# Kernel optimization log

Hardware: AMD Instinct MI355X
Metric: run time of the kernel (lower is better)

Reference implementation:

```python
import jax, jax.numpy as jnp
import numpy as np

B, N, D, O = 16384, 784, 8, 10   # batch, num_sites, bond_dim, output_dim
LABEL = N // 2                   # 392
L_LEFT = LABEL - 1               # sites 1..391 -> 391 mid tensors
L_RIGHT = N - 2 - LABEL          # sites 393..782 -> 390 mid tensors


def setup_inputs() -> dict:
    key = jax.random.key(0)
    k0, k1, k2, k3, k4, k5 = jax.random.split(key, 6)
    x = jax.random.uniform(k0, (B, N, 1), dtype=jnp.float32)
    # scale mid tensors so the 784-site matrix product stays O(1):
    # per-site variance multiplier ~ D * var(w) * E[phi^2]*2 with E[phi^2]=1/3
    s_mid = (3.0 / (2.0 * D)) ** 0.5
    w0 = jax.random.normal(k1, (2, D), dtype=jnp.float32) * 1.2
    W_left = jax.random.normal(k2, (L_LEFT, D, 2, D), dtype=jnp.float32) * s_mid
    w_label = jax.random.normal(k3, (D, 2, D, O), dtype=jnp.float32) * s_mid
    W_right = jax.random.normal(k4, (L_RIGHT, D, 2, D), dtype=jnp.float32) * s_mid
    w_last = jax.random.normal(k5, (D, 2), dtype=jnp.float32) * 1.2
    return {"x": x, "w0": w0, "W_left": W_left, "w_label": w_label,
            "W_right": W_right, "w_last": w_last}


def reference(x, w0, W_left, w_label, W_right, w_last):
    p = jnp.squeeze(x, axis=-1)                       # [B, N]
    phi = jnp.stack([1.0 - p, p], axis=-1)            # [B, N, 2] feature map

    # site 0: [B,2] x [2,D] -> left boundary vector [B,D]
    v = jnp.einsum('bf,fd->bd', phi[:, 0], w0)

    def step_left(v, xw):
        phi_i, w_i = xw                               # [B,2], [D,2,D]
        return jnp.einsum('bd,dfe,bf->be', v, w_i, phi_i), None

    phiL = jnp.transpose(phi[:, 1:LABEL], (1, 0, 2))  # [L_LEFT, B, 2]
    v, _ = jax.lax.scan(step_left, v, (phiL, W_left))

    # label site: [B,D] x [D,2,D,O] x [B,2] -> [B,D,O]
    v = jnp.einsum('bd,dfeo,bf->beo', v, w_label, phi[:, LABEL])

    def step_right(v, xw):
        phi_i, w_i = xw
        return jnp.einsum('bdo,dfe,bf->beo', v, w_i, phi_i), None

    phiR = jnp.transpose(phi[:, LABEL + 1:N - 1], (1, 0, 2))  # [L_RIGHT, B, 2]
    v, _ = jax.lax.scan(step_right, v, (phiR, W_right))

    # last site: right boundary vector [B,D], then close the chain -> [B,O]
    r = jnp.einsum('bf,df->bd', phi[:, N - 1], w_last)
    return jnp.einsum('bdo,bd->bo', v, r)
```

## Files before the change

### kernel.cpp

```cpp
#include <hip/hip_runtime.h>


#define NSITES 784
#define DIM    8
#define ODIM   10
#define LABEL  392
#define WST    160
#define XST    20

#define QP_X1 0xB1
#define QP_X2 0x4E
#define QP_X3 0x1B
#define RHM   0x141

template <int CTRL>
__device__ __forceinline__ float dppf(float v) {
    const int vi = __float_as_int(v);
    return __int_as_float(__builtin_amdgcn_update_dpp(vi, vi, CTRL, 0xF, 0xF, false));
}

__device__ __forceinline__ float site_step(float v, float p, const float* wsite) {
    const float4 w00 = *(const float4*)(wsite + 0);
    const float4 w01 = *(const float4*)(wsite + 4);
    const float4 w10 = *(const float4*)(wsite + 8);
    const float4 w11 = *(const float4*)(wsite + 12);
    const float t1 = dppf<QP_X1>(v);
    const float t2 = dppf<QP_X2>(v);
    const float t3 = dppf<QP_X3>(v);
    const float t7 = dppf<RHM>(v);
    const float t6 = dppf<QP_X1>(t7);
    const float t5 = dppf<QP_X2>(t7);
    const float t4 = dppf<QP_X3>(t7);
    float a0 = v * w00.x;
    float a1 = v * w10.x;
    a0 = fmaf(t1, w00.y, a0);  a1 = fmaf(t1, w10.y, a1);
    a0 = fmaf(t2, w00.z, a0);  a1 = fmaf(t2, w10.z, a1);
    a0 = fmaf(t3, w00.w, a0);  a1 = fmaf(t3, w10.w, a1);
    a0 = fmaf(t4, w01.x, a0);  a1 = fmaf(t4, w11.x, a1);
    a0 = fmaf(t5, w01.y, a0);  a1 = fmaf(t5, w11.y, a1);
    a0 = fmaf(t6, w01.z, a0);  a1 = fmaf(t6, w11.z, a1);
    a0 = fmaf(t7, w01.w, a0);  a1 = fmaf(t7, w11.w, a1);
    return fmaf(1.0f - p, a0, p * a1);
}

__global__ __launch_bounds__(512, 4) void mps_fused(
    const float* __restrict__ x,
    const float* __restrict__ w0,
    const float* __restrict__ Wl,
    const float* __restrict__ wlab,
    const float* __restrict__ Wr,
    const float* __restrict__ wlast,
    float* __restrict__ out)
{
    __shared__ float wb[2][2][16 * WST];
    __shared__ float xb[2][2][32 * XST];
    __shared__ float wl[1280];
    __shared__ float vout[2][256];

    const int tid  = threadIdx.x;
    const int side = tid >> 8;
    const int stid = tid & 255;
    const int g    = stid >> 3;
    const int e    = stid & 7;
    const int b0   = blockIdx.x * 32;

    if (tid < 320)
        *(float4*)&wl[tid * 4] = *(const float4*)&wlab[tid * 4];

    auto stage = [&](int bufi, int c, int nt) {
        float* wdst = wb[side][bufi];
        float* xdst = xb[side][bufi];
        if (side == 0) {
            #pragma unroll
            for (int r = 0; r < 2; ++r) {
                const int cid = stid + 256 * r;
                const int s   = cid >> 5;
                const int u   = cid & 31;
                const int d   = u >> 2;
                const int f   = (u >> 1) & 1;
                const int e0  = (u & 1) * 4;
                if (s < nt) {
                    const float4 w = *(const float4*)(Wl + (size_t)(c * 16 + s) * 128 + d * 16 + f * 8 + e0);
                    float* dst = wdst + s * WST + f * 8;
                    dst[(e0 + 0) * 20 + ((e0 + 0) ^ d)] = w.x;
                    dst[(e0 + 1) * 20 + ((e0 + 1) ^ d)] = w.y;
                    dst[(e0 + 2) * 20 + ((e0 + 2) ^ d)] = w.z;
                    dst[(e0 + 3) * 20 + ((e0 + 3) ^ d)] = w.w;
                }
            }
            #pragma unroll
            for (int r = 0; r < 2; ++r) {
                const int cid = stid + 256 * r;
                const int s   = cid >> 5;
                const int g2  = cid & 31;
                if (s < nt)
                    xdst[g2 * XST + s] = x[(size_t)(b0 + g2) * NSITES + 1 + c * 16 + s];
            }
        } else {
            #pragma unroll
            for (int r = 0; r < 2; ++r) {
                const int cid = stid + 256 * r;
                const int s   = cid >> 5;
                const int u   = cid & 31;
                const int d   = u >> 2;
                const int k   = u & 3;
                const int f   = k >> 1;
                const int e0  = (k & 1) * 4;
                if (s < nt) {
                    const float4 w = *(const float4*)(Wr + (size_t)(389 - c * 16 - s) * 128 + u * 4);
                    float* dst = wdst + s * WST + d * 20 + f * 8;
                    dst[(e0 + 0) ^ d] = w.x;
                    dst[(e0 + 1) ^ d] = w.y;
                    dst[(e0 + 2) ^ d] = w.z;
                    dst[(e0 + 3) ^ d] = w.w;
                }
            }
            #pragma unroll
            for (int r = 0; r < 2; ++r) {
                const int cid = stid + 256 * r;
                const int s   = cid >> 5;
                const int g2  = cid & 31;
                if (s < nt)
                    xdst[g2 * XST + s] = x[(size_t)(b0 + g2) * NSITES + 782 - c * 16 - s];
            }
        }
    };

    float v;
    if (side == 0) {
        const float p = x[(size_t)(b0 + g) * NSITES + 0];
        v = fmaf(1.0f - p, w0[e], p * w0[DIM + e]);
    } else {
        const float p = x[(size_t)(b0 + g) * NSITES + (NSITES - 1)];
        v = fmaf(1.0f - p, wlast[e * 2], p * wlast[e * 2 + 1]);
    }

    stage(0, 0, 16);
    int buf = 0;

    const float* wp0 = &wb[side][0][e * 20];
    const float* wp1 = &wb[side][1][e * 20];
    const float* xp0 = &xb[side][0][g * XST];
    const float* xp1 = &xb[side][1][g * XST];

    #pragma unroll 1
    for (int c = 0; c < 24; ++c) {
        __syncthreads();
        if (c < 23) stage(buf ^ 1, c + 1, 16);
        else        stage(buf ^ 1, 24, side == 0 ? 7 : 6);
        const float* wp = buf ? wp1 : wp0;
        const float* xp = buf ? xp1 : xp0;
        #pragma unroll
        for (int jb = 0; jb < 4; ++jb) {
            const float4 xq = *(const float4*)(xp + jb * 4);
            #pragma unroll
            for (int jj = 0; jj < 4; ++jj) {
                const int   j = jb * 4 + jj;
                const float p = (jj == 0) ? xq.x : (jj == 1) ? xq.y : (jj == 2) ? xq.z : xq.w;
                v = site_step(v, p, wp + j * WST);
            }
        }
        buf ^= 1;
    }

    __syncthreads();
    {
        const int nt = side == 0 ? 7 : 6;
        const float* wp = buf ? wp1 : wp0;
        const float* xp = buf ? xp1 : xp0;
        for (int j = 0; j < nt; ++j)
            v = site_step(v, xp[j], wp + j * WST);
    }

    vout[side][stid] = v;
    __syncthreads();

    if (tid < 320) {
        const int bl = tid / 10;
        const int o  = tid - bl * 10;
        const float p = x[(size_t)(b0 + bl) * NSITES + LABEL];
        const float q = 1.0f - p;
        const float* vl = &vout[0][bl * 8];
        const float* rv = &vout[1][bl * 8];
        float acc = 0.0f;
        #pragma unroll
        for (int d = 0; d < DIM; ++d) {
            const float vld = vl[d];
            #pragma unroll
            for (int ee = 0; ee < DIM; ++ee) {
                const float m = fmaf(q, wl[((d * 2 + 0) * DIM + ee) * ODIM + o],
                                     p * wl[((d * 2 + 1) * DIM + ee) * ODIM + o]);
                acc = fmaf(vld * rv[ee], m, acc);
            }
        }
        out[(size_t)(b0 + bl) * ODIM + o] = acc;
    }
}

extern "C" void kernel_launch(void* const* d_in, const int* in_sizes, int n_in,
                              void* d_out, int out_size, void* d_ws, size_t ws_size,
                              hipStream_t stream) {
    const float* x     = (const float*)d_in[0];
    const float* w0    = (const float*)d_in[1];
    const float* Wl    = (const float*)d_in[2];
    const float* wlab  = (const float*)d_in[3];
    const float* Wr    = (const float*)d_in[4];
    const float* wlast = (const float*)d_in[5];

    mps_fused<<<512, 512, 0, stream>>>(x, w0, Wl, wlab, Wr, wlast, (float*)d_out);
}
```

Measured before the change: 185.2 us.

## Process four batch rows per thread and prefetch stages through registers

Each thread now carries four independent chain vectors (64 batch rows per block, 256 threads, 256 blocks), so the site weights loaded from shared memory are reused across four rows and the four DPP/FMA chains can interleave to hide latency. The global loads for the next stage go into registers before the compute and are written to shared memory after it, which overlaps memory traffic with arithmetic. The final interpolation is rewritten as a single fma form. The cost is fewer resident threads per CU (launch bounds 256,1 and only 256 blocks) and more register pressure, so occupancy and latency hiding across waves drop.

```diff
diff --git a/kernel.cpp b/kernel.cpp
--- a/kernel.cpp
+++ b/kernel.cpp
@@ -6,6 +6,7 @@
 #define ODIM   10
 #define LABEL  392
 #define WST    160
+#define CST    20
 #define XST    20
 
 #define QP_X1 0xB1
@@ -19,11 +20,9 @@
     return __int_as_float(__builtin_amdgcn_update_dpp(vi, vi, CTRL, 0xF, 0xF, false));
 }
 
-__device__ __forceinline__ float site_step(float v, float p, const float* wsite) {
-    const float4 w00 = *(const float4*)(wsite + 0);
-    const float4 w01 = *(const float4*)(wsite + 4);
-    const float4 w10 = *(const float4*)(wsite + 8);
-    const float4 w11 = *(const float4*)(wsite + 12);
+struct W4 { float4 w00, w01, w10, w11; };
+
+__device__ __forceinline__ float site_step(float v, float p, const W4& w) {
     const float t1 = dppf<QP_X1>(v);
     const float t2 = dppf<QP_X2>(v);
     const float t3 = dppf<QP_X3>(v);
@@ -31,19 +30,19 @@
     const float t6 = dppf<QP_X1>(t7);
     const float t5 = dppf<QP_X2>(t7);
     const float t4 = dppf<QP_X3>(t7);
-    float a0 = v * w00.x;
-    float a1 = v * w10.x;
-    a0 = fmaf(t1, w00.y, a0);  a1 = fmaf(t1, w10.y, a1);
-    a0 = fmaf(t2, w00.z, a0);  a1 = fmaf(t2, w10.z, a1);
-    a0 = fmaf(t3, w00.w, a0);  a1 = fmaf(t3, w10.w, a1);
-    a0 = fmaf(t4, w01.x, a0);  a1 = fmaf(t4, w11.x, a1);
-    a0 = fmaf(t5, w01.y, a0);  a1 = fmaf(t5, w11.y, a1);
-    a0 = fmaf(t6, w01.z, a0);  a1 = fmaf(t6, w11.z, a1);
-    a0 = fmaf(t7, w01.w, a0);  a1 = fmaf(t7, w11.w, a1);
-    return fmaf(1.0f - p, a0, p * a1);
-}
-
-__global__ __launch_bounds__(512, 4) void mps_fused(
+    float a0 = v * w.w00.x;
+    float a1 = v * w.w10.x;
+    a0 = fmaf(t1, w.w00.y, a0);  a1 = fmaf(t1, w.w10.y, a1);
+    a0 = fmaf(t2, w.w00.z, a0);  a1 = fmaf(t2, w.w10.z, a1);
+    a0 = fmaf(t3, w.w00.w, a0);  a1 = fmaf(t3, w.w10.w, a1);
+    a0 = fmaf(t4, w.w01.x, a0);  a1 = fmaf(t4, w.w11.x, a1);
+    a0 = fmaf(t5, w.w01.y, a0);  a1 = fmaf(t5, w.w11.y, a1);
+    a0 = fmaf(t6, w.w01.z, a0);  a1 = fmaf(t6, w.w11.z, a1);
+    a0 = fmaf(t7, w.w01.w, a0);  a1 = fmaf(t7, w.w11.w, a1);
+    return fmaf(p, a1 - a0, a0);
+}
+
+__global__ __launch_bounds__(256, 1) void mps_fused(
     const float* __restrict__ x,
     const float* __restrict__ w0,
     const float* __restrict__ Wl,
@@ -53,131 +52,204 @@
     float* __restrict__ out)
 {
     __shared__ float wb[2][2][16 * WST];
-    __shared__ float xb[2][2][32 * XST];
+    __shared__ float xb[2][2][64 * XST];
     __shared__ float wl[1280];
-    __shared__ float vout[2][256];
+    __shared__ float vout[2][512];
 
     const int tid  = threadIdx.x;
-    const int side = tid >> 8;
-    const int stid = tid & 255;
-    const int g    = stid >> 3;
-    const int e    = stid & 7;
-    const int b0   = blockIdx.x * 32;
-
-    if (tid < 320)
-        *(float4*)&wl[tid * 4] = *(const float4*)&wlab[tid * 4];
-
-    auto stage = [&](int bufi, int c, int nt) {
+    const int side = tid >> 7;
+    const int stid = tid & 127;
+    const int w    = stid >> 6;
+    const int lane = stid & 63;
+    const int g    = lane >> 3;
+    const int e    = lane & 7;
+    const int b0   = blockIdx.x * 64;
+
+    for (int k = tid; k < 320; k += 256)
+        *(float4*)&wl[k * 4] = *(const float4*)&wlab[k * 4];
+
+    float4 wr[4];
+    float  xr[8];
+
+    auto stage_load = [&](int c, int nt) {
+        if (side == 0) {
+            #pragma unroll
+            for (int r = 0; r < 4; ++r) {
+                const int cid = stid + 128 * r;
+                const int s   = cid >> 5;
+                const int u   = cid & 31;
+                if (s < nt)
+                    wr[r] = *(const float4*)(Wl + (size_t)(c * 16 + s) * 128
+                                             + (u >> 2) * 16 + ((u >> 1) & 1) * 8 + (u & 1) * 4);
+            }
+            #pragma unroll
+            for (int r = 0; r < 8; ++r) {
+                const int cid = stid + 128 * r;
+                const int bl  = cid >> 4;
+                const int sx  = cid & 15;
+                if (sx < nt)
+                    xr[r] = x[(size_t)(b0 + bl) * NSITES + 1 + c * 16 + sx];
+            }
+        } else {
+            #pragma unroll
+            for (int r = 0; r < 4; ++r) {
+                const int cid = stid + 128 * r;
+                const int s   = cid >> 5;
+                const int u   = cid & 31;
+                if (s < nt)
+                    wr[r] = *(const float4*)(Wr + (size_t)(389 - c * 16 - s) * 128 + u * 4);
+            }
+            #pragma unroll
+            for (int r = 0; r < 8; ++r) {
+                const int cid = stid + 128 * r;
+                const int bl  = cid >> 4;
+                const int sx  = cid & 15;
+                if (sx < nt)
+                    xr[r] = x[(size_t)(b0 + bl) * NSITES + 782 - c * 16 - sx];
+            }
+        }
+    };
+
+    auto stage_write = [&](int bufi, int nt) {
         float* wdst = wb[side][bufi];
         float* xdst = xb[side][bufi];
         if (side == 0) {
             #pragma unroll
-            for (int r = 0; r < 2; ++r) {
-                const int cid = stid + 256 * r;
+            for (int r = 0; r < 4; ++r) {
+                const int cid = stid + 128 * r;
                 const int s   = cid >> 5;
                 const int u   = cid & 31;
                 const int d   = u >> 2;
                 const int f   = (u >> 1) & 1;
                 const int e0  = (u & 1) * 4;
                 if (s < nt) {
-                    const float4 w = *(const float4*)(Wl + (size_t)(c * 16 + s) * 128 + d * 16 + f * 8 + e0);
                     float* dst = wdst + s * WST + f * 8;
-                    dst[(e0 + 0) * 20 + ((e0 + 0) ^ d)] = w.x;
-                    dst[(e0 + 1) * 20 + ((e0 + 1) ^ d)] = w.y;
-                    dst[(e0 + 2) * 20 + ((e0 + 2) ^ d)] = w.z;
-                    dst[(e0 + 3) * 20 + ((e0 + 3) ^ d)] = w.w;
+                    dst[(e0 + 0) * CST + ((e0 + 0) ^ d)] = wr[r].x;
+                    dst[(e0 + 1) * CST + ((e0 + 1) ^ d)] = wr[r].y;
+                    dst[(e0 + 2) * CST + ((e0 + 2) ^ d)] = wr[r].z;
+                    dst[(e0 + 3) * CST + ((e0 + 3) ^ d)] = wr[r].w;
                 }
             }
-            #pragma unroll
-            for (int r = 0; r < 2; ++r) {
-                const int cid = stid + 256 * r;
-                const int s   = cid >> 5;
-                const int g2  = cid & 31;
-                if (s < nt)
-                    xdst[g2 * XST + s] = x[(size_t)(b0 + g2) * NSITES + 1 + c * 16 + s];
-            }
         } else {
             #pragma unroll
-            for (int r = 0; r < 2; ++r) {
-                const int cid = stid + 256 * r;
+            for (int r = 0; r < 4; ++r) {
+                const int cid = stid + 128 * r;
                 const int s   = cid >> 5;
                 const int u   = cid & 31;
                 const int d   = u >> 2;
-                const int k   = u & 3;
-                const int f   = k >> 1;
-                const int e0  = (k & 1) * 4;
+                const int k2  = u & 3;
+                const int f   = k2 >> 1;
+                const int e0  = (k2 & 1) * 4;
                 if (s < nt) {
-                    const float4 w = *(const float4*)(Wr + (size_t)(389 - c * 16 - s) * 128 + u * 4);
-                    float* dst = wdst + s * WST + d * 20 + f * 8;
-                    dst[(e0 + 0) ^ d] = w.x;
-                    dst[(e0 + 1) ^ d] = w.y;
-                    dst[(e0 + 2) ^ d] = w.z;
-                    dst[(e0 + 3) ^ d] = w.w;
+                    float* dst = wdst + s * WST + d * CST + f * 8;
+                    dst[(e0 + 0) ^ d] = wr[r].x;
+                    dst[(e0 + 1) ^ d] = wr[r].y;
+                    dst[(e0 + 2) ^ d] = wr[r].z;
+                    dst[(e0 + 3) ^ d] = wr[r].w;
                 }
             }
-            #pragma unroll
-            for (int r = 0; r < 2; ++r) {
-                const int cid = stid + 256 * r;
-                const int s   = cid >> 5;
-                const int g2  = cid & 31;
-                if (s < nt)
-                    xdst[g2 * XST + s] = x[(size_t)(b0 + g2) * NSITES + 782 - c * 16 - s];
-            }
+        }
+        #pragma unroll
+        for (int r = 0; r < 8; ++r) {
+            const int cid = stid + 128 * r;
+            const int bl  = cid >> 4;
+            const int sx  = cid & 15;
+            if (sx < nt)
+                xdst[bl * XST + sx] = xr[r];
         }
     };
 
-    float v;
+    float vv[4];
     if (side == 0) {
-        const float p = x[(size_t)(b0 + g) * NSITES + 0];
-        v = fmaf(1.0f - p, w0[e], p * w0[DIM + e]);
+        #pragma unroll
+        for (int k = 0; k < 4; ++k) {
+            const int bl  = w * 32 + k * 8 + g;
+            const float p = x[(size_t)(b0 + bl) * NSITES];
+            vv[k] = fmaf(1.0f - p, w0[e], p * w0[DIM + e]);
+        }
     } else {
-        const float p = x[(size_t)(b0 + g) * NSITES + (NSITES - 1)];
-        v = fmaf(1.0f - p, wlast[e * 2], p * wlast[e * 2 + 1]);
-    }
-
-    stage(0, 0, 16);
+        #pragma unroll
+        for (int k = 0; k < 4; ++k) {
+            const int bl  = w * 32 + k * 8 + g;
+            const float p = x[(size_t)(b0 + bl) * NSITES + (NSITES - 1)];
+            vv[k] = fmaf(1.0f - p, wlast[e * 2], p * wlast[e * 2 + 1]);
+        }
+    }
+
+    const int nt_tail = side ? 6 : 7;
+
+    stage_load(0, 16);
+    stage_write(0, 16);
     int buf = 0;
 
-    const float* wp0 = &wb[side][0][e * 20];
-    const float* wp1 = &wb[side][1][e * 20];
-    const float* xp0 = &xb[side][0][g * XST];
-    const float* xp1 = &xb[side][1][g * XST];
+    auto compute16 = [&](int bufi) {
+        const float* wp = &wb[side][bufi][e * CST];
+        const float* xp = &xb[side][bufi][(w * 32 + g) * XST];
+        #pragma unroll
+        for (int jb = 0; jb < 4; ++jb) {
+            float4 xq[4];
+            #pragma unroll
+            for (int k = 0; k < 4; ++k)
+                xq[k] = *(const float4*)(xp + k * 8 * XST + jb * 4);
+            #pragma unroll
+            for (int jj = 0; jj < 4; ++jj) {
+                const int j = jb * 4 + jj;
+                W4 wv;
+                wv.w00 = *(const float4*)(wp + j * WST + 0);
+                wv.w01 = *(const float4*)(wp + j * WST + 4);
+                wv.w10 = *(const float4*)(wp + j * WST + 8);
+                wv.w11 = *(const float4*)(wp + j * WST + 12);
+                #pragma unroll
+                for (int k = 0; k < 4; ++k) {
+                    const float p = (jj == 0) ? xq[k].x : (jj == 1) ? xq[k].y
+                                  : (jj == 2) ? xq[k].z : xq[k].w;
+                    vv[k] = site_step(vv[k], p, wv);
+                }
+            }
+        }
+    };
 
     #pragma unroll 1
-    for (int c = 0; c < 24; ++c) {
+    for (int c = 0; c < 23; ++c) {
         __syncthreads();
-        if (c < 23) stage(buf ^ 1, c + 1, 16);
-        else        stage(buf ^ 1, 24, side == 0 ? 7 : 6);
-        const float* wp = buf ? wp1 : wp0;
-        const float* xp = buf ? xp1 : xp0;
-        #pragma unroll
-        for (int jb = 0; jb < 4; ++jb) {
-            const float4 xq = *(const float4*)(xp + jb * 4);
-            #pragma unroll
-            for (int jj = 0; jj < 4; ++jj) {
-                const int   j = jb * 4 + jj;
-                const float p = (jj == 0) ? xq.x : (jj == 1) ? xq.y : (jj == 2) ? xq.z : xq.w;
-                v = site_step(v, p, wp + j * WST);
-            }
-        }
+        stage_load(c + 1, 16);
+        compute16(buf);
+        __builtin_amdgcn_sched_barrier(0);
+        stage_write(buf ^ 1, 16);
         buf ^= 1;
     }
+
+    __syncthreads();
+    stage_load(24, nt_tail);
+    compute16(buf);
+    __builtin_amdgcn_sched_barrier(0);
+    stage_write(buf ^ 1, nt_tail);
+    buf ^= 1;
 
     __syncthreads();
     {
-        const int nt = side == 0 ? 7 : 6;
-        const float* wp = buf ? wp1 : wp0;
-        const float* xp = buf ? xp1 : xp0;
-        for (int j = 0; j < nt; ++j)
-            v = site_step(v, xp[j], wp + j * WST);
-    }
-
-    vout[side][stid] = v;
+        const float* wp = &wb[side][buf][e * CST];
+        const float* xp = &xb[side][buf][(w * 32 + g) * XST];
+        for (int j = 0; j < nt_tail; ++j) {
+            W4 wv;
+            wv.w00 = *(const float4*)(wp + j * WST + 0);
+            wv.w01 = *(const float4*)(wp + j * WST + 4);
+            wv.w10 = *(const float4*)(wp + j * WST + 8);
+            wv.w11 = *(const float4*)(wp + j * WST + 12);
+            #pragma unroll
+            for (int k = 0; k < 4; ++k)
+                vv[k] = site_step(vv[k], xp[k * 8 * XST + j], wv);
+        }
+    }
+
+    #pragma unroll
+    for (int k = 0; k < 4; ++k)
+        vout[side][(w * 32 + k * 8 + g) * 8 + e] = vv[k];
     __syncthreads();
 
-    if (tid < 320) {
-        const int bl = tid / 10;
-        const int o  = tid - bl * 10;
+    for (int idx = tid; idx < 640; idx += 256) {
+        const int bl = idx / 10;
+        const int o  = idx - bl * 10;
         const float p = x[(size_t)(b0 + bl) * NSITES + LABEL];
         const float q = 1.0f - p;
         const float* vl = &vout[0][bl * 8];
@@ -200,6 +272,7 @@
 extern "C" void kernel_launch(void* const* d_in, const int* in_sizes, int n_in,
                               void* d_out, int out_size, void* d_ws, size_t ws_size,
                               hipStream_t stream) {
+    (void)in_sizes; (void)n_in; (void)d_ws; (void)ws_size; (void)out_size;
     const float* x     = (const float*)d_in[0];
     const float* w0    = (const float*)d_in[1];
     const float* Wl    = (const float*)d_in[2];
@@ -207,5 +280,5 @@
     const float* Wr    = (const float*)d_in[4];
     const float* wlast = (const float*)d_in[5];
 
-    mps_fused<<<512, 512, 0, stream>>>(x, w0, Wl, wlab, Wr, wlast, (float*)d_out);
-}
+    mps_fused<<<256, 256, 0, stream>>>(x, w0, Wl, wlab, Wr, wlast, (float*)d_out);
+}
```

Result: slower. 195.6 us (+5.6%).

## Process two batch rows per thread with packed FP32 math and register-staged prefetch

Applied to the files above, without the earlier changes.

Each thread now carries two batch rows in a float2 and uses v_pk_mul/v_pk_fma packed FP32 instructions. Weights are duplicated into pairs in shared memory so one packed operand serves both rows. Global loads for the next chunk go into registers before compute and are written to LDS afterwards, separated by a sched_barrier, to overlap memory latency with the serial chain. Blocks now cover 64 rows (grid halved, launch bounds 512,2), which doubles the DPP work per thread and the LDS footprint and may reduce occupancy.

```diff
diff --git a/kernel.cpp b/kernel.cpp
--- a/kernel.cpp
+++ b/kernel.cpp
@@ -5,45 +5,75 @@
 #define DIM    8
 #define ODIM   10
 #define LABEL  392
-#define WST    160
-#define XST    20
-
-#define QP_X1 0xB1
-#define QP_X2 0x4E
-#define QP_X3 0x1B
-#define RHM   0x141
-
-template <int CTRL>
-__device__ __forceinline__ float dppf(float v) {
-    const int vi = __float_as_int(v);
-    return __int_as_float(__builtin_amdgcn_update_dpp(vi, vi, CTRL, 0xF, 0xF, false));
-}
-
-__device__ __forceinline__ float site_step(float v, float p, const float* wsite) {
-    const float4 w00 = *(const float4*)(wsite + 0);
-    const float4 w01 = *(const float4*)(wsite + 4);
-    const float4 w10 = *(const float4*)(wsite + 8);
-    const float4 w11 = *(const float4*)(wsite + 12);
-    const float t1 = dppf<QP_X1>(v);
-    const float t2 = dppf<QP_X2>(v);
-    const float t3 = dppf<QP_X3>(v);
-    const float t7 = dppf<RHM>(v);
-    const float t6 = dppf<QP_X1>(t7);
-    const float t5 = dppf<QP_X2>(t7);
-    const float t4 = dppf<QP_X3>(t7);
-    float a0 = v * w00.x;
-    float a1 = v * w10.x;
-    a0 = fmaf(t1, w00.y, a0);  a1 = fmaf(t1, w10.y, a1);
-    a0 = fmaf(t2, w00.z, a0);  a1 = fmaf(t2, w10.z, a1);
-    a0 = fmaf(t3, w00.w, a0);  a1 = fmaf(t3, w10.w, a1);
-    a0 = fmaf(t4, w01.x, a0);  a1 = fmaf(t4, w11.x, a1);
-    a0 = fmaf(t5, w01.y, a0);  a1 = fmaf(t5, w11.y, a1);
-    a0 = fmaf(t6, w01.z, a0);  a1 = fmaf(t6, w11.z, a1);
-    a0 = fmaf(t7, w01.w, a0);  a1 = fmaf(t7, w11.w, a1);
-    return fmaf(1.0f - p, a0, p * a1);
-}
-
-__global__ __launch_bounds__(512, 4) void mps_fused(
+#define WST2   288
+#define CST2   36
+#define XQST   34
+
+typedef float v2f __attribute__((ext_vector_type(2)));
+
+__device__ __forceinline__ float dpp_x1(float s) {
+    float d; asm("v_mov_b32_dpp %0, %1 quad_perm:[1,0,3,2] row_mask:0xf bank_mask:0xf"
+                 : "=v"(d) : "v"(s)); return d;
+}
+__device__ __forceinline__ float dpp_x2(float s) {
+    float d; asm("v_mov_b32_dpp %0, %1 quad_perm:[2,3,0,1] row_mask:0xf bank_mask:0xf"
+                 : "=v"(d) : "v"(s)); return d;
+}
+__device__ __forceinline__ float dpp_x3(float s) {
+    float d; asm("v_mov_b32_dpp %0, %1 quad_perm:[3,2,1,0] row_mask:0xf bank_mask:0xf"
+                 : "=v"(d) : "v"(s)); return d;
+}
+__device__ __forceinline__ float dpp_x7(float s) {
+    float d; asm("v_mov_b32_dpp %0, %1 row_half_mirror row_mask:0xf bank_mask:0xf"
+                 : "=v"(d) : "v"(s)); return d;
+}
+
+__device__ __forceinline__ v2f pk_mul(v2f a, v2f b) {
+    v2f d; asm("v_pk_mul_f32 %0, %1, %2" : "=v"(d) : "v"(a), "v"(b)); return d;
+}
+__device__ __forceinline__ v2f pk_fma(v2f a, v2f b, v2f c) {
+    v2f d; asm("v_pk_fma_f32 %0, %1, %2, %3" : "=v"(d) : "v"(a), "v"(b), "v"(c)); return d;
+}
+__device__ __forceinline__ v2f pk_add(v2f a, v2f b) {
+    v2f d; asm("v_pk_add_f32 %0, %1, %2" : "=v"(d) : "v"(a), "v"(b)); return d;
+}
+
+__device__ __forceinline__ v2f XY(const float4& q) { v2f r = {q.x, q.y}; return r; }
+__device__ __forceinline__ v2f ZW(const float4& q) { v2f r = {q.z, q.w}; return r; }
+
+__device__ __forceinline__ v2f site_step2(v2f v, v2f p, const float* wc) {
+    const float4 q0 = *(const float4*)(wc + 0);
+    const float4 q1 = *(const float4*)(wc + 4);
+    const float4 q2 = *(const float4*)(wc + 8);
+    const float4 q3 = *(const float4*)(wc + 12);
+    const float4 q4 = *(const float4*)(wc + 16);
+    const float4 q5 = *(const float4*)(wc + 20);
+    const float4 q6 = *(const float4*)(wc + 24);
+    const float4 q7 = *(const float4*)(wc + 28);
+    v2f t1; t1.x = dpp_x1(v.x); t1.y = dpp_x1(v.y);
+    v2f t2; t2.x = dpp_x2(v.x); t2.y = dpp_x2(v.y);
+    v2f t3; t3.x = dpp_x3(v.x); t3.y = dpp_x3(v.y);
+    v2f t7; t7.x = dpp_x7(v.x); t7.y = dpp_x7(v.y);
+    v2f t6; t6.x = dpp_x1(t7.x); t6.y = dpp_x1(t7.y);
+    v2f t5; t5.x = dpp_x2(t7.x); t5.y = dpp_x2(t7.y);
+    v2f t4; t4.x = dpp_x3(t7.x); t4.y = dpp_x3(t7.y);
+    v2f a00 = pk_mul(v,  XY(q0)); a00 = pk_fma(t1, ZW(q0), a00);
+    a00 = pk_fma(t2, XY(q1), a00); a00 = pk_fma(t3, ZW(q1), a00);
+    v2f a01 = pk_mul(t4, XY(q2)); a01 = pk_fma(t5, ZW(q2), a01);
+    a01 = pk_fma(t6, XY(q3), a01); a01 = pk_fma(t7, ZW(q3), a01);
+    v2f a10 = pk_mul(v,  XY(q4)); a10 = pk_fma(t1, ZW(q4), a10);
+    a10 = pk_fma(t2, XY(q5), a10); a10 = pk_fma(t3, ZW(q5), a10);
+    v2f a11 = pk_mul(t4, XY(q6)); a11 = pk_fma(t5, ZW(q6), a11);
+    a11 = pk_fma(t6, XY(q7), a11); a11 = pk_fma(t7, ZW(q7), a11);
+    const v2f a0 = pk_add(a00, a01);
+    const v2f a1 = pk_add(a10, a11);
+    v2f r;
+    r.x = fmaf(p.x, a1.x - a0.x, a0.x);
+    r.y = fmaf(p.y, a1.y - a0.y, a0.y);
+    return r;
+}
+
+__global__ __launch_bounds__(512, 2) void mps_fused(
     const float* __restrict__ x,
     const float* __restrict__ w0,
     const float* __restrict__ Wl,
@@ -52,132 +82,164 @@
     const float* __restrict__ wlast,
     float* __restrict__ out)
 {
-    __shared__ float wb[2][2][16 * WST];
-    __shared__ float xb[2][2][32 * XST];
+    __shared__ float wb[2][2][16 * WST2];
+    __shared__ float xb[2][2][32 * XQST];
     __shared__ float wl[1280];
-    __shared__ float vout[2][256];
-
-    const int tid  = threadIdx.x;
-    const int side = tid >> 8;
-    const int stid = tid & 255;
-    const int g    = stid >> 3;
-    const int e    = stid & 7;
-    const int b0   = blockIdx.x * 32;
+    __shared__ float vout[2][512];
+
+    const int tid   = threadIdx.x;
+    const int side  = tid >> 8;
+    const int stid2 = tid & 255;
+    const int w     = stid2 >> 6;
+    const int lane  = stid2 & 63;
+    const int g     = lane >> 3;
+    const int e     = lane & 7;
+    const int pr    = w * 8 + g;
+    const int b0    = blockIdx.x * 64;
 
     if (tid < 320)
         *(float4*)&wl[tid * 4] = *(const float4*)&wlab[tid * 4];
 
-    auto stage = [&](int bufi, int c, int nt) {
+    float4 wr[2];
+    float  xr[4];
+
+    auto stage_load = [&](int c, int nt) {
+        const float* W = side == 0 ? Wl : Wr;
+        #pragma unroll
+        for (int r = 0; r < 2; ++r) {
+            const int cid = stid2 + 256 * r;
+            const int s   = cid >> 5;
+            const int u   = cid & 31;
+            if (s < nt) {
+                const int row = side == 0 ? (c * 16 + s) : (389 - c * 16 - s);
+                wr[r] = *(const float4*)(W + (size_t)row * 128 + u * 4);
+            }
+        }
+        #pragma unroll
+        for (int r = 0; r < 4; ++r) {
+            const int cid = stid2 + 256 * r;
+            const int bl  = cid >> 4;
+            const int sx  = cid & 15;
+            if (sx < nt) {
+                const int col = side == 0 ? (1 + c * 16 + sx) : (782 - c * 16 - sx);
+                xr[r] = x[(size_t)(b0 + bl) * NSITES + col];
+            }
+        }
+    };
+
+    auto stage_write = [&](int bufi, int nt) {
         float* wdst = wb[side][bufi];
         float* xdst = xb[side][bufi];
-        if (side == 0) {
-            #pragma unroll
-            for (int r = 0; r < 2; ++r) {
-                const int cid = stid + 256 * r;
-                const int s   = cid >> 5;
-                const int u   = cid & 31;
-                const int d   = u >> 2;
-                const int f   = (u >> 1) & 1;
-                const int e0  = (u & 1) * 4;
-                if (s < nt) {
-                    const float4 w = *(const float4*)(Wl + (size_t)(c * 16 + s) * 128 + d * 16 + f * 8 + e0);
-                    float* dst = wdst + s * WST + f * 8;
-                    dst[(e0 + 0) * 20 + ((e0 + 0) ^ d)] = w.x;
-                    dst[(e0 + 1) * 20 + ((e0 + 1) ^ d)] = w.y;
-                    dst[(e0 + 2) * 20 + ((e0 + 2) ^ d)] = w.z;
-                    dst[(e0 + 3) * 20 + ((e0 + 3) ^ d)] = w.w;
+        #pragma unroll
+        for (int r = 0; r < 2; ++r) {
+            const int cid = stid2 + 256 * r;
+            const int s   = cid >> 5;
+            const int u   = cid & 31;
+            const int d   = u >> 2;
+            const int f   = (u >> 1) & 1;
+            const int e0  = (u & 1) * 4;
+            if (s < nt) {
+                if (side == 0) {
+                    float* dst = wdst + s * WST2 + f * 16;
+                    v2f c0 = {wr[r].x, wr[r].x};
+                    v2f c1 = {wr[r].y, wr[r].y};
+                    v2f c2 = {wr[r].z, wr[r].z};
+                    v2f c3 = {wr[r].w, wr[r].w};
+                    *(v2f*)(dst + (e0 + 0) * CST2 + ((e0 + 0) ^ d) * 2) = c0;
+                    *(v2f*)(dst + (e0 + 1) * CST2 + ((e0 + 1) ^ d) * 2) = c1;
+                    *(v2f*)(dst + (e0 + 2) * CST2 + ((e0 + 2) ^ d) * 2) = c2;
+                    *(v2f*)(dst + (e0 + 3) * CST2 + ((e0 + 3) ^ d) * 2) = c3;
+                } else {
+                    float* dst = wdst + s * WST2 + d * CST2 + f * 16;
+                    v2f c0 = {wr[r].x, wr[r].x};
+                    v2f c1 = {wr[r].y, wr[r].y};
+                    v2f c2 = {wr[r].z, wr[r].z};
+                    v2f c3 = {wr[r].w, wr[r].w};
+                    *(v2f*)(dst + ((e0 + 0) ^ d) * 2) = c0;
+                    *(v2f*)(dst + ((e0 + 1) ^ d) * 2) = c1;
+                    *(v2f*)(dst + ((e0 + 2) ^ d) * 2) = c2;
+                    *(v2f*)(dst + ((e0 + 3) ^ d) * 2) = c3;
                 }
             }
-            #pragma unroll
-            for (int r = 0; r < 2; ++r) {
-                const int cid = stid + 256 * r;
-                const int s   = cid >> 5;
-                const int g2  = cid & 31;
-                if (s < nt)
-                    xdst[g2 * XST + s] = x[(size_t)(b0 + g2) * NSITES + 1 + c * 16 + s];
-            }
-        } else {
-            #pragma unroll
-            for (int r = 0; r < 2; ++r) {
-                const int cid = stid + 256 * r;
-                const int s   = cid >> 5;
-                const int u   = cid & 31;
-                const int d   = u >> 2;
-                const int k   = u & 3;
-                const int f   = k >> 1;
-                const int e0  = (k & 1) * 4;
-                if (s < nt) {
-                    const float4 w = *(const float4*)(Wr + (size_t)(389 - c * 16 - s) * 128 + u * 4);
-                    float* dst = wdst + s * WST + d * 20 + f * 8;
-                    dst[(e0 + 0) ^ d] = w.x;
-                    dst[(e0 + 1) ^ d] = w.y;
-                    dst[(e0 + 2) ^ d] = w.z;
-                    dst[(e0 + 3) ^ d] = w.w;
-                }
-            }
-            #pragma unroll
-            for (int r = 0; r < 2; ++r) {
-                const int cid = stid + 256 * r;
-                const int s   = cid >> 5;
-                const int g2  = cid & 31;
-                if (s < nt)
-                    xdst[g2 * XST + s] = x[(size_t)(b0 + g2) * NSITES + 782 - c * 16 - s];
-            }
+        }
+        #pragma unroll
+        for (int r = 0; r < 4; ++r) {
+            const int cid  = stid2 + 256 * r;
+            const int bl   = cid >> 4;
+            const int sx   = cid & 15;
+            const int prw  = bl >> 1;
+            const int half = bl & 1;
+            if (sx < nt)
+                xdst[prw * XQST + sx * 2 + half] = xr[r];
         }
     };
 
-    float v;
+    v2f vv;
     if (side == 0) {
-        const float p = x[(size_t)(b0 + g) * NSITES + 0];
-        v = fmaf(1.0f - p, w0[e], p * w0[DIM + e]);
+        const float p0 = x[(size_t)(b0 + 2 * pr + 0) * NSITES];
+        const float p1 = x[(size_t)(b0 + 2 * pr + 1) * NSITES];
+        vv.x = fmaf(1.0f - p0, w0[e], p0 * w0[DIM + e]);
+        vv.y = fmaf(1.0f - p1, w0[e], p1 * w0[DIM + e]);
     } else {
-        const float p = x[(size_t)(b0 + g) * NSITES + (NSITES - 1)];
-        v = fmaf(1.0f - p, wlast[e * 2], p * wlast[e * 2 + 1]);
-    }
-
-    stage(0, 0, 16);
+        const float p0 = x[(size_t)(b0 + 2 * pr + 0) * NSITES + (NSITES - 1)];
+        const float p1 = x[(size_t)(b0 + 2 * pr + 1) * NSITES + (NSITES - 1)];
+        vv.x = fmaf(1.0f - p0, wlast[e * 2], p0 * wlast[e * 2 + 1]);
+        vv.y = fmaf(1.0f - p1, wlast[e * 2], p1 * wlast[e * 2 + 1]);
+    }
+
+    const int nt_tail = side ? 6 : 7;
+
+    stage_load(0, 16);
+    stage_write(0, 16);
     int buf = 0;
 
-    const float* wp0 = &wb[side][0][e * 20];
-    const float* wp1 = &wb[side][1][e * 20];
-    const float* xp0 = &xb[side][0][g * XST];
-    const float* xp1 = &xb[side][1][g * XST];
+    auto compute16 = [&](int bufi) {
+        const float* wp = &wb[side][bufi][e * CST2];
+        const float* xp = &xb[side][bufi][pr * XQST];
+        #pragma unroll
+        for (int jh = 0; jh < 8; ++jh) {
+            const float4 xq = *(const float4*)(xp + jh * 4);
+            v2f pa; pa.x = xq.x; pa.y = xq.y;
+            v2f pb; pb.x = xq.z; pb.y = xq.w;
+            vv = site_step2(vv, pa, wp + (2 * jh + 0) * WST2);
+            vv = site_step2(vv, pb, wp + (2 * jh + 1) * WST2);
+        }
+    };
 
     #pragma unroll 1
-    for (int c = 0; c < 24; ++c) {
+    for (int c = 0; c < 23; ++c) {
         __syncthreads();
-        if (c < 23) stage(buf ^ 1, c + 1, 16);
-        else        stage(buf ^ 1, 24, side == 0 ? 7 : 6);
-        const float* wp = buf ? wp1 : wp0;
-        const float* xp = buf ? xp1 : xp0;
-        #pragma unroll
-        for (int jb = 0; jb < 4; ++jb) {
-            const float4 xq = *(const float4*)(xp + jb * 4);
-            #pragma unroll
-            for (int jj = 0; jj < 4; ++jj) {
-                const int   j = jb * 4 + jj;
-                const float p = (jj == 0) ? xq.x : (jj == 1) ? xq.y : (jj == 2) ? xq.z : xq.w;
-                v = site_step(v, p, wp + j * WST);
-            }
-        }
+        stage_load(c + 1, 16);
+        compute16(buf);
+        __builtin_amdgcn_sched_barrier(0);
+        stage_write(buf ^ 1, 16);
         buf ^= 1;
     }
+
+    __syncthreads();
+    stage_load(24, nt_tail);
+    compute16(buf);
+    __builtin_amdgcn_sched_barrier(0);
+    stage_write(buf ^ 1, nt_tail);
+    buf ^= 1;
 
     __syncthreads();
     {
-        const int nt = side == 0 ? 7 : 6;
-        const float* wp = buf ? wp1 : wp0;
-        const float* xp = buf ? xp1 : xp0;
-        for (int j = 0; j < nt; ++j)
-            v = site_step(v, xp[j], wp + j * WST);
-    }
-
-    vout[side][stid] = v;
+        const float* wp = &wb[side][buf][e * CST2];
+        const float* xp = &xb[side][buf][pr * XQST];
+        for (int j = 0; j < nt_tail; ++j) {
+            v2f p; p.x = xp[j * 2]; p.y = xp[j * 2 + 1];
+            vv = site_step2(vv, p, wp + j * WST2);
+        }
+    }
+
+    vout[side][(2 * pr + 0) * 8 + e] = vv.x;
+    vout[side][(2 * pr + 1) * 8 + e] = vv.y;
     __syncthreads();
 
-    if (tid < 320) {
-        const int bl = tid / 10;
-        const int o  = tid - bl * 10;
+    for (int idx = tid; idx < 640; idx += 512) {
+        const int bl = idx / 10;
+        const int o  = idx - bl * 10;
         const float p = x[(size_t)(b0 + bl) * NSITES + LABEL];
         const float q = 1.0f - p;
         const float* vl = &vout[0][bl * 8];
@@ -200,6 +262,7 @@
 extern "C" void kernel_launch(void* const* d_in, const int* in_sizes, int n_in,
                               void* d_out, int out_size, void* d_ws, size_t ws_size,
                               hipStream_t stream) {
+    (void)in_sizes; (void)n_in; (void)d_ws; (void)ws_size; (void)out_size;
     const float* x     = (const float*)d_in[0];
     const float* w0    = (const float*)d_in[1];
     const float* Wl    = (const float*)d_in[2];
@@ -207,5 +270,5 @@
     const float* Wr    = (const float*)d_in[4];
     const float* wlast = (const float*)d_in[5];
 
-    mps_fused<<<512, 512, 0, stream>>>(x, w0, Wl, wlab, Wr, wlast, (float*)d_out);
-}
+    mps_fused<<<256, 512, 0, stream>>>(x, w0, Wl, wlab, Wr, wlast, (float*)d_out);
+}
```

Measured after the change: 163.6 us. 1.13x faster.
